# Kernel optimization log

Measured on AMD Instinct MI355X. Metric: run time of the kernel, lower is better.

Reference implementation:

```python
import jax
import jax.numpy as jnp
import numpy as np

NPOINT = 512
RADIUS = 0.2
K = 32


def setup_inputs() -> dict:
    key = jax.random.key(0)
    k1, k2 = jax.random.split(key)
    xyz = jax.random.uniform(k1, (8, 16384, 3), dtype=jnp.float32)      # [B,N,3] in unit cube
    features = jax.random.normal(k2, (8, 128, 16384), dtype=jnp.float32)  # [B,D,N]
    return {"xyz": xyz, "features": features}


def farthest_point_sample(xyz, npoint):
    # xyz: [B,N,3] -> centroids [B,npoint] int32. Deterministic start at index 0
    # (the torch code does randint(...)*0).
    B, N, _ = xyz.shape
    init_dist = jnp.full((B, N), 1e10, dtype=xyz.dtype)
    init_far = jnp.zeros((B,), dtype=jnp.int32)

    def step(carry, _):
        distance, farthest = carry
        centroid = jnp.take_along_axis(xyz, farthest[:, None, None], axis=1)  # [B,1,3]
        d = jnp.sum((xyz - centroid) ** 2, axis=-1)                           # [B,N]
        distance = jnp.minimum(distance, d)
        new_far = jnp.argmax(distance, axis=-1).astype(jnp.int32)
        return (distance, new_far), farthest

    (_, _), cents = jax.lax.scan(step, (init_dist, init_far), None, length=npoint)
    return cents.T  # [B, npoint]


def square_distance(src, dst):
    # src [B,S,3], dst [B,N,3] -> [B,S,N]
    d = -2.0 * jnp.einsum("bsc,bnc->bsn", src, dst)
    d = d + jnp.sum(src ** 2, -1)[:, :, None]
    d = d + jnp.sum(dst ** 2, -1)[:, None, :]
    return d


def query_ball_point(radius, nsample, xyz, new_xyz):
    B, N, _ = xyz.shape
    sqrd = square_distance(new_xyz, xyz)                              # [B,S,N]
    arangeN = jnp.arange(N, dtype=jnp.int32)[None, None, :]
    idx = jnp.where(sqrd > radius ** 2, N, arangeN)                   # out-of-ball -> sentinel N
    idx = jnp.sort(idx, axis=-1)[:, :, :nsample]                      # [B,S,K]
    first = idx[:, :, :1]
    idx = jnp.where(idx == N, first, idx)                             # pad with first valid neighbor
    return idx


def index_points(points, idx):
    # points [B,N,C], idx [B,...] -> [B,...,C]
    B = points.shape[0]
    bidx = jnp.arange(B).reshape((B,) + (1,) * (idx.ndim - 1))
    return points[bidx, idx]


def reference(xyz, features):
    # xyz [B,N,3], features [B,D,N]
    cent = farthest_point_sample(xyz, NPOINT)                 # [B,S]
    new_xyz = index_points(xyz, cent)                         # [B,S,3]
    idx = query_ball_point(RADIUS, K, xyz, new_xyz)           # [B,S,K]
    pts = jnp.transpose(features, (0, 2, 1))                  # [B,N,D]
    grouped = index_points(pts, idx)                          # [B,S,K,D]
    sub_features = jnp.max(grouped, axis=2)                   # [B,S,D]  (max over K neighbors)
    sub_features = jnp.transpose(sub_features, (0, 2, 1))     # [B,D,S]
    return new_xyz, sub_features
```

## Files before the change

kernel.cpp:

```cpp
#include <hip/hip_runtime.h>
#include <stdint.h>
#include <math.h>

#define NB      8
#define NPTS    16384
#define NPOINT  512
#define NCH     128
#define KNBR    32
#define R2      0.04f

#define FPS_THR 512
#define PPT     32
#define QBLKS   512

#define CENT_OFF 0
#define MAP_OFF  16384

#define DPP_ARG_STEP(v, p, CTRL) do {                                          \
    float _ov = __builtin_bit_cast(float, __builtin_amdgcn_update_dpp(         \
        __builtin_bit_cast(int, (v)), __builtin_bit_cast(int, (v)),            \
        (CTRL), 0xF, 0xF, false));                                             \
    int _op = __builtin_amdgcn_update_dpp((p), (p), (CTRL), 0xF, 0xF, false);  \
    bool _t = (_ov > (v)) || ((_ov == (v)) && (_op < (p)));                    \
    (v) = _t ? _ov : (v);                                                      \
    (p) = _t ? _op : (p);                                                      \
} while (0)

__device__ __forceinline__ int cell_of(float x, float y, float z) {
    int cx = (int)(x * 8.0f); cx = cx < 0 ? 0 : (cx > 7 ? 7 : cx);
    int cy = (int)(y * 8.0f); cy = cy < 0 ? 0 : (cy > 7 ? 7 : cy);
    int cz = (int)(z * 8.0f); cz = cz < 0 ? 0 : (cz > 7 ? 7 : cz);
    int m = 0;
    m |= ((cx & 1) << 2) | ((cx & 2) << 4) | ((cx & 4) << 6);
    m |= ((cy & 1) << 1) | ((cy & 2) << 3) | ((cy & 4) << 5);
    m |=  (cz & 1)       | ((cz & 2) << 2) | ((cz & 4) << 4);
    return m;
}

__global__
__attribute__((amdgpu_flat_work_group_size(FPS_THR, FPS_THR)))
__attribute__((amdgpu_waves_per_eu(2, 4)))
void fps_query_kernel(const float* __restrict__ xyz,
                      const float* __restrict__ feat,
                      float* __restrict__ out,
                      int* __restrict__ cent,
                      int* __restrict__ map,
                      float* __restrict__ out_sub)
{
    const int blk = blockIdx.x;
    const int tid = threadIdx.x;
    const int lane = tid & 63;
    const int wid  = tid >> 6;

    if (blk < NB) {
        const int b = blk;
        const float* xb = xyz + (size_t)b * NPTS * 3;
        int* gmap = map + b * NPTS;

        __shared__ int   s_hist[512];
        __shared__ float s_meta[8][PPT][4];
        __shared__ float s_v[2][8];
        __shared__ int   s_p[2][8];

        s_hist[tid] = 0;
        __syncthreads();
        for (int k = 0; k < PPT; ++k) {
            int p = k * FPS_THR + tid;
            int c = cell_of(xb[p * 3 + 0], xb[p * 3 + 1], xb[p * 3 + 2]);
            atomicAdd(&s_hist[c], 1);
        }
        __syncthreads();
        int mycount = s_hist[tid];
        for (int off = 1; off < 512; off <<= 1) {
            int v = (tid >= off) ? s_hist[tid - off] : 0;
            __syncthreads();
            s_hist[tid] += v;
            __syncthreads();
        }
        int excl = s_hist[tid] - mycount;
        __syncthreads();
        s_hist[tid] = excl;
        __syncthreads();
        for (int k = 0; k < PPT; ++k) {
            int p = k * FPS_THR + tid;
            int c = cell_of(xb[p * 3 + 0], xb[p * 3 + 1], xb[p * 3 + 2]);
            int pos = atomicAdd(&s_hist[c], 1);
            gmap[pos] = p;
        }
        __threadfence_block();
        __syncthreads();
        float px[PPT], py[PPT], pz[PPT], d[PPT];
        int   idx[PPT];
#pragma unroll
        for (int k = 0; k < PPT; ++k) {
            int pos = (k * 8 + wid) * 64 + lane;
            int op  = gmap[pos];
            idx[k] = op;
            px[k] = xb[op * 3 + 0];
            py[k] = xb[op * 3 + 1];
            pz[k] = xb[op * 3 + 2];
            d[k]  = 1e10f;
        }
#pragma unroll
        for (int k = 0; k < PPT; ++k) {
            float mnx = px[k], mxx = px[k];
            float mny = py[k], mxy = py[k];
            float mnz = pz[k], mxz = pz[k];
#pragma unroll
            for (int s = 1; s < 64; s <<= 1) {
                mnx = fminf(mnx, __shfl_xor(mnx, s, 64));
                mxx = fmaxf(mxx, __shfl_xor(mxx, s, 64));
                mny = fminf(mny, __shfl_xor(mny, s, 64));
                mxy = fmaxf(mxy, __shfl_xor(mxy, s, 64));
                mnz = fminf(mnz, __shfl_xor(mnz, s, 64));
                mxz = fmaxf(mxz, __shfl_xor(mxz, s, 64));
            }
            if (lane == 0) {
                float hx = (mxx - mnx) * 0.5f;
                float hy = (mxy - mny) * 0.5f;
                float hz = (mxz - mnz) * 0.5f;
                s_meta[wid][k][0] = (mnx + mxx) * 0.5f;
                s_meta[wid][k][1] = (mny + mxy) * 0.5f;
                s_meta[wid][k][2] = (mnz + mxz) * 0.5f;
                s_meta[wid][k][3] =
                    sqrtf(hx * hx + hy * hy + hz * hz) * 1.0001f + 1e-6f;
            }
        }
        __syncthreads();
        const float bmx = s_meta[wid][lane & 31][0];
        const float bmy = s_meta[wid][lane & 31][1];
        const float bmz = s_meta[wid][lane & 31][2];
        const float br  = s_meta[wid][lane & 31][3];
        float U = 1e10f;

        float cx = xb[0], cy = xb[1], cz = xb[2];
        if (tid == 0) {
            out[((size_t)b * NPOINT + 0) * 3 + 0] = cx;
            out[((size_t)b * NPOINT + 0) * 3 + 1] = cy;
            out[((size_t)b * NPOINT + 0) * 3 + 2] = cz;
            __hip_atomic_store(&cent[b * NPOINT + 0], 0,
                               __ATOMIC_RELAXED, __HIP_MEMORY_SCOPE_AGENT);
        }

        for (int i = 1; i < NPOINT; ++i) {
            float dcx = cx - bmx, dcy = cy - bmy, dcz = cz - bmz;
            float dc  = sqrtf(dcx * dcx + dcy * dcy + dcz * dcz);
            float t   = dc - br;
            bool skip = (t > 0.0f) && (t * t >= U + 2e-5f);
            unsigned mask = (unsigned)__ballot(skip);

            if (mask != 0xFFFFFFFFu) {
#pragma unroll
                for (int k = 0; k < PPT; ++k) {
                    if (!(mask & (1u << k))) {
                        float dx = __fsub_rn(px[k], cx);
                        float dy = __fsub_rn(py[k], cy);
                        float dz = __fsub_rn(pz[k], cz);
                        float dd = __fadd_rn(__fadd_rn(__fmul_rn(dx, dx),
                                                       __fmul_rn(dy, dy)),
                                             __fmul_rn(dz, dz));
                        d[k] = fminf(d[k], dd);
                    }
                }
            }
            if (!((mask >> (lane & 31)) & 1u)) {
                float ub = dc + br;
                U = fminf(U, ub * ub * 1.0001f + 1e-6f);
            }
            float vmax = d[0];
#pragma unroll
            for (int k = 1; k < PPT; ++k) vmax = fmaxf(vmax, d[k]);
            int bi = idx[PPT - 1];
#pragma unroll
            for (int k = PPT - 2; k >= 0; --k) bi = (d[k] == vmax) ? idx[k] : bi;

            float rv = vmax;
            int   rp = bi;
            DPP_ARG_STEP(rv, rp, 0xB1);
            DPP_ARG_STEP(rv, rp, 0x4E);
            DPP_ARG_STEP(rv, rp, 0x141);
            DPP_ARG_STEP(rv, rp, 0x140);
            DPP_ARG_STEP(rv, rp, 0x142);
            DPP_ARG_STEP(rv, rp, 0x143);
            const int par = i & 1;
            if (lane == 63) { s_v[par][wid] = rv; s_p[par][wid] = rp; }
            __syncthreads();
            float fv = s_v[par][lane & 7];
            int   fp = s_p[par][lane & 7];
            DPP_ARG_STEP(fv, fp, 0xB1);
            DPP_ARG_STEP(fv, fp, 0x4E);
            DPP_ARG_STEP(fv, fp, 0x141);
            const int cur = __builtin_amdgcn_readfirstlane(fp);
            cx = xb[cur * 3 + 0];
            cy = xb[cur * 3 + 1];
            cz = xb[cur * 3 + 2];
            if (tid == 0) {
                size_t o = ((size_t)b * NPOINT + i) * 3;
                out[o + 0] = cx; out[o + 1] = cy; out[o + 2] = cz;
                __hip_atomic_store(&cent[b * NPOINT + i], cur,
                                   __ATOMIC_RELAXED, __HIP_MEMORY_SCOPE_AGENT);
            }
        }
    } else {
        __shared__ int lidx[8][KNBR];
        const int wv = (blk - NB) * 8 + wid;
        const int b  = wv >> 9;
        const int s  = wv & 511;
        const float* xb = xyz + (size_t)b * NPTS * 3;

        int ci;
        for (;;) {
            ci = __hip_atomic_load(&cent[b * NPOINT + s],
                                   __ATOMIC_RELAXED, __HIP_MEMORY_SCOPE_AGENT);
            if (ci >= 0) break;
            __builtin_amdgcn_s_sleep(8);
        }

        const float sx = xb[ci * 3 + 0];
        const float sy = xb[ci * 3 + 1];
        const float sz = xb[ci * 3 + 2];
        const float snorm = __fadd_rn(__fadd_rn(__fmul_rn(sx, sx),
                                                __fmul_rn(sy, sy)),
                                      __fmul_rn(sz, sz));

        int found = 0;
        for (int base = 0; base < NPTS && found < KNBR; base += 64) {
            int j = base + lane;
            float dx = xb[j * 3 + 0];
            float dy = xb[j * 3 + 1];
            float dz = xb[j * 3 + 2];
            float dn = __fadd_rn(__fadd_rn(__fmul_rn(dx, dx),
                                           __fmul_rn(dy, dy)),
                                 __fmul_rn(dz, dz));
            float dot = __fadd_rn(__fadd_rn(__fmul_rn(sx, dx),
                                            __fmul_rn(sy, dy)),
                                  __fmul_rn(sz, dz));
            float dqp = __fadd_rn(__fadd_rn(__fmul_rn(-2.0f, dot), snorm), dn);
            bool inball = !(dqp > R2);
            unsigned long long m = __ballot(inball);
            int before = (int)__popcll(m & ((1ULL << lane) - 1ULL));
            int slot = found + before;
            if (inball && slot < KNBR) lidx[wid][slot] = j;
            found += (int)__popcll(m);
        }
        int cnt = found < KNBR ? found : KNBR;

        float a0 = -INFINITY, a1 = -INFINITY;
        const float* fb = feat + (size_t)b * NCH * NPTS;
        for (int m = 0; m < cnt; ++m) {
            int i = lidx[wid][m];
            a0 = fmaxf(a0, fb[(size_t)lane * NPTS + i]);
            a1 = fmaxf(a1, fb[(size_t)(lane + 64) * NPTS + i]);
        }
        out_sub[((size_t)b * NCH + lane) * NPOINT + s] = a0;
        out_sub[((size_t)b * NCH + lane + 64) * NPOINT + s] = a1;
    }
}

extern "C" void kernel_launch(void* const* d_in, const int* in_sizes, int n_in,
                              void* d_out, int out_size, void* d_ws, size_t ws_size,
                              hipStream_t stream)
{
    const float* xyz  = (const float*)d_in[0];
    const float* feat = (const float*)d_in[1];
    float* out = (float*)d_out;

    int* cent = (int*)((char*)d_ws + CENT_OFF);
    int* map  = (int*)((char*)d_ws + MAP_OFF);

    hipMemsetAsync((char*)d_ws + CENT_OFF, 0xFF, NB * NPOINT * 4, stream);

    hipLaunchKernelGGL(fps_query_kernel, dim3(NB + QBLKS), dim3(FPS_THR), 0,
                       stream, xyz, feat, out, cent, map,
                       out + (size_t)NB * NPOINT * 3);
}
```

Baseline: 1.037 ms.

## Make query waves persistent with grid-stride loop over fixed block count

Query blocks become persistent: a fixed grid of 256 blocks (8 FPS + 248 query) loops over all centroid tasks in stride order instead of launching one wave per centroid. The occupancy hint is pinned to 2 waves per EU, centroid indices are published before writing the output coordinates, and feature gathers and output stores use nontemporal hints. The aim is to stop query blocks from occupying CUs while they spin on unpublished centroids, which could slow the FPS blocks, and to keep streaming feature reads from polluting cache. The risk is that fewer query waves leaves less parallelism to drain the tail after FPS finishes.

```diff
diff --git a/kernel.cpp b/kernel.cpp
--- a/kernel.cpp
+++ b/kernel.cpp
@@ -11,7 +11,8 @@
 
 #define FPS_THR 512
 #define PPT     32
-#define QBLKS   512
+#define NBLK    256
+#define NQW     ((NBLK - NB) * 8)
 
 #define CENT_OFF 0
 #define MAP_OFF  16384
@@ -39,7 +40,7 @@
 
 __global__
 __attribute__((amdgpu_flat_work_group_size(FPS_THR, FPS_THR)))
-__attribute__((amdgpu_waves_per_eu(2, 4)))
+__attribute__((amdgpu_waves_per_eu(2, 2)))
 void fps_query_kernel(const float* __restrict__ xyz,
                       const float* __restrict__ feat,
                       float* __restrict__ out,
@@ -135,11 +136,11 @@
 
         float cx = xb[0], cy = xb[1], cz = xb[2];
         if (tid == 0) {
+            __hip_atomic_store(&cent[b * NPOINT + 0], 0,
+                               __ATOMIC_RELAXED, __HIP_MEMORY_SCOPE_AGENT);
             out[((size_t)b * NPOINT + 0) * 3 + 0] = cx;
             out[((size_t)b * NPOINT + 0) * 3 + 1] = cy;
             out[((size_t)b * NPOINT + 0) * 3 + 2] = cz;
-            __hip_atomic_store(&cent[b * NPOINT + 0], 0,
-                               __ATOMIC_RELAXED, __HIP_MEMORY_SCOPE_AGENT);
         }
 
         for (int i = 1; i < NPOINT; ++i) {
@@ -195,65 +196,74 @@
             cy = xb[cur * 3 + 1];
             cz = xb[cur * 3 + 2];
             if (tid == 0) {
+                __hip_atomic_store(&cent[b * NPOINT + i], cur,
+                                   __ATOMIC_RELAXED, __HIP_MEMORY_SCOPE_AGENT);
                 size_t o = ((size_t)b * NPOINT + i) * 3;
                 out[o + 0] = cx; out[o + 1] = cy; out[o + 2] = cz;
-                __hip_atomic_store(&cent[b * NPOINT + i], cur,
-                                   __ATOMIC_RELAXED, __HIP_MEMORY_SCOPE_AGENT);
             }
         }
     } else {
         __shared__ int lidx[8][KNBR];
-        const int wv = (blk - NB) * 8 + wid;
-        const int b  = wv >> 9;
-        const int s  = wv & 511;
-        const float* xb = xyz + (size_t)b * NPTS * 3;
-
-        int ci;
-        for (;;) {
-            ci = __hip_atomic_load(&cent[b * NPOINT + s],
-                                   __ATOMIC_RELAXED, __HIP_MEMORY_SCOPE_AGENT);
-            if (ci >= 0) break;
-            __builtin_amdgcn_s_sleep(8);
-        }
-
-        const float sx = xb[ci * 3 + 0];
-        const float sy = xb[ci * 3 + 1];
-        const float sz = xb[ci * 3 + 2];
-        const float snorm = __fadd_rn(__fadd_rn(__fmul_rn(sx, sx),
-                                                __fmul_rn(sy, sy)),
-                                      __fmul_rn(sz, sz));
-
-        int found = 0;
-        for (int base = 0; base < NPTS && found < KNBR; base += 64) {
-            int j = base + lane;
-            float dx = xb[j * 3 + 0];
-            float dy = xb[j * 3 + 1];
-            float dz = xb[j * 3 + 2];
-            float dn = __fadd_rn(__fadd_rn(__fmul_rn(dx, dx),
-                                           __fmul_rn(dy, dy)),
-                                 __fmul_rn(dz, dz));
-            float dot = __fadd_rn(__fadd_rn(__fmul_rn(sx, dx),
-                                            __fmul_rn(sy, dy)),
-                                  __fmul_rn(sz, dz));
-            float dqp = __fadd_rn(__fadd_rn(__fmul_rn(-2.0f, dot), snorm), dn);
-            bool inball = !(dqp > R2);
-            unsigned long long m = __ballot(inball);
-            int before = (int)__popcll(m & ((1ULL << lane) - 1ULL));
-            int slot = found + before;
-            if (inball && slot < KNBR) lidx[wid][slot] = j;
-            found += (int)__popcll(m);
-        }
-        int cnt = found < KNBR ? found : KNBR;
-
-        float a0 = -INFINITY, a1 = -INFINITY;
-        const float* fb = feat + (size_t)b * NCH * NPTS;
-        for (int m = 0; m < cnt; ++m) {
-            int i = lidx[wid][m];
-            a0 = fmaxf(a0, fb[(size_t)lane * NPTS + i]);
-            a1 = fmaxf(a1, fb[(size_t)(lane + 64) * NPTS + i]);
-        }
-        out_sub[((size_t)b * NCH + lane) * NPOINT + s] = a0;
-        out_sub[((size_t)b * NCH + lane + 64) * NPOINT + s] = a1;
+        const int qw = (blk - NB) * 8 + wid;
+
+        for (int t = qw; t < NB * NPOINT; t += NQW) {
+            const int b = t >> 9;
+            const int s = t & 511;
+            const float* xb = xyz + (size_t)b * NPTS * 3;
+
+            int ci;
+            for (;;) {
+                ci = __hip_atomic_load(&cent[b * NPOINT + s],
+                                       __ATOMIC_RELAXED,
+                                       __HIP_MEMORY_SCOPE_AGENT);
+                if (ci >= 0) break;
+                __builtin_amdgcn_s_sleep(8);
+            }
+
+            const float sx = xb[ci * 3 + 0];
+            const float sy = xb[ci * 3 + 1];
+            const float sz = xb[ci * 3 + 2];
+            const float snorm = __fadd_rn(__fadd_rn(__fmul_rn(sx, sx),
+                                                    __fmul_rn(sy, sy)),
+                                          __fmul_rn(sz, sz));
+
+            int found = 0;
+            for (int base = 0; base < NPTS && found < KNBR; base += 64) {
+                int j = base + lane;
+                float dx = xb[j * 3 + 0];
+                float dy = xb[j * 3 + 1];
+                float dz = xb[j * 3 + 2];
+                float dn = __fadd_rn(__fadd_rn(__fmul_rn(dx, dx),
+                                               __fmul_rn(dy, dy)),
+                                     __fmul_rn(dz, dz));
+                float dot = __fadd_rn(__fadd_rn(__fmul_rn(sx, dx),
+                                                __fmul_rn(sy, dy)),
+                                      __fmul_rn(sz, dz));
+                float dqp = __fadd_rn(__fadd_rn(__fmul_rn(-2.0f, dot), snorm),
+                                      dn);
+                bool inball = !(dqp > R2);
+                unsigned long long m = __ballot(inball);
+                int before = (int)__popcll(m & ((1ULL << lane) - 1ULL));
+                int slot = found + before;
+                if (inball && slot < KNBR) lidx[wid][slot] = j;
+                found += (int)__popcll(m);
+            }
+            int cnt = found < KNBR ? found : KNBR;
+
+            float a0 = -INFINITY, a1 = -INFINITY;
+            const float* fb = feat + (size_t)b * NCH * NPTS;
+            for (int m = 0; m < cnt; ++m) {
+                int i = lidx[wid][m];
+                a0 = fmaxf(a0, __builtin_nontemporal_load(
+                                   &fb[(size_t)lane * NPTS + i]));
+                a1 = fmaxf(a1, __builtin_nontemporal_load(
+                                   &fb[(size_t)(lane + 64) * NPTS + i]));
+            }
+            __builtin_nontemporal_store(
+                a0, &out_sub[((size_t)b * NCH + lane) * NPOINT + s]);
+            __builtin_nontemporal_store(
+                a1, &out_sub[((size_t)b * NCH + lane + 64) * NPOINT + s]);
+        }
     }
 }
 
@@ -270,7 +280,7 @@
 
     hipMemsetAsync((char*)d_ws + CENT_OFF, 0xFF, NB * NPOINT * 4, stream);
 
-    hipLaunchKernelGGL(fps_query_kernel, dim3(NB + QBLKS), dim3(FPS_THR), 0,
+    hipLaunchKernelGGL(fps_query_kernel, dim3(NBLK), dim3(FPS_THR), 0,
                        stream, xyz, feat, out, cent, map,
                        out + (size_t)NB * NPOINT * 3);
 }
```

Result: slower. 1.071 ms (+3.3%).
